# Kernel optimization log

Hardware: AMD Instinct MI355X
Metric: run time of the kernel (lower is better)

Reference implementation:

```python
import jax, jax.numpy as jnp
import numpy as np

B, L, T, H, NL, DFF, DIN = 4096, 64, 256, 8, 4, 1024, 6
HD = T // H
EPS = 1e-9


def setup_inputs() -> dict:
    key = jax.random.key(0)
    ks = jax.random.split(key, 12)
    s = 0.02
    inp = {
        "link_states": jax.random.uniform(ks[0], (B, L, DIN), jnp.float32) * 10.0,
        "link_W1": jax.random.normal(ks[1], (L, DIN, T), jnp.float32) * s,
        "link_b1": jnp.zeros((L, T), jnp.float32),
        "link_W2": jax.random.normal(ks[2], (L, T, T), jnp.float32) * s,
        "link_b2": jnp.zeros((L, T), jnp.float32),
        "Wqkv": jax.random.normal(ks[3], (NL, 3 * T, T), jnp.float32) * s,
        "bqkv": jnp.zeros((NL, 3 * T), jnp.float32),
        "Wo": jax.random.normal(ks[4], (NL, T, T), jnp.float32) * s,
        "bo": jnp.zeros((NL, T), jnp.float32),
        "ln1_g": jnp.ones((NL, T), jnp.float32),
        "ln1_b": jnp.zeros((NL, T), jnp.float32),
        "Wff1": jax.random.normal(ks[5], (NL, DFF, T), jnp.float32) * s,
        "bff1": jnp.zeros((NL, DFF), jnp.float32),
        "Wff2": jax.random.normal(ks[6], (NL, T, DFF), jnp.float32) * s,
        "bff2": jnp.zeros((NL, T), jnp.float32),
        "ln2_g": jnp.ones((NL, T), jnp.float32),
        "ln2_b": jnp.zeros((NL, T), jnp.float32),
        "head_W1": jax.random.normal(ks[7], (T, T), jnp.float32) * s,
        "head_b1": jnp.zeros((T,), jnp.float32),
        "head_W2": jax.random.normal(ks[8], (T, 1), jnp.float32) * s,
        "head_b2": jnp.zeros((1,), jnp.float32),
    }
    return inp


def _layernorm(x, g, b):
    m = x.mean(-1, keepdims=True)
    v = ((x - m) ** 2).mean(-1, keepdims=True)
    return (x - m) * jax.lax.rsqrt(v + 1e-5) * g + b


def _normalize_inputs(x):
    # x: [B, L, 6]
    prop = jnp.clip(x[:, :, 0], 0.0)
    tx = jnp.clip(x[:, :, 1], 0.0)
    sum_pt = prop + tx
    # torch.median returns lower-middle element for even L
    t_ref = jnp.sort(sum_pt, axis=1)[:, (L - 1) // 2][:, None]
    t_ref = jnp.clip(t_ref, 1e-6)
    f0 = prop / t_ref
    f1 = tx / t_ref
    f2 = x[:, :, 2]
    f3 = jnp.log1p(jnp.clip(x[:, :, 3], 0.0))
    f4 = jnp.log1p(jnp.clip(x[:, :, 4], 0.0) / t_ref)
    f5 = jnp.log1p(jnp.clip(x[:, :, 5], 0.0))
    head5 = jnp.stack([f0, f1, f2, f3, f4], axis=-1)  # [B,L,5]
    mean_a = head5.mean(axis=1, keepdims=True)
    std_a = head5.std(axis=1, keepdims=True) + EPS
    head5 = jnp.clip(head5, mean_a - 3.0 * std_a, mean_a + 3.0 * std_a)
    mean = head5.mean(axis=1, keepdims=True)
    std = head5.std(axis=1, keepdims=True) + EPS
    head5 = (head5 - mean) / std
    return jnp.concatenate([head5, f5[:, :, None]], axis=-1)


def _posenc():
    pos = jnp.arange(L, dtype=jnp.float32)[:, None]
    div = jnp.exp(-jnp.log(10000.0) * jnp.arange(0, T, 2, dtype=jnp.float32) / T)
    pe = jnp.zeros((L, T), jnp.float32)
    pe = pe.at[:, 0::2].set(jnp.sin(pos * div))
    pe = pe.at[:, 1::2].set(jnp.cos(pos * div))
    return pe


def _forward(link_states, link_W1, link_b1, link_W2, link_b2, Wqkv, bqkv, Wo, bo,
             ln1_g, ln1_b, Wff1, bff1, Wff2, bff2, ln2_g, ln2_b,
             head_W1, head_b1, head_W2, head_b2):
    x = _normalize_inputs(link_states)  # [B,L,6]
    # per-link (unshared) MLP encoders, batched as grouped matmuls
    h = jax.nn.relu(jnp.einsum('bld,ldt->blt', x, link_W1) + link_b1)
    tok = jnp.einsum('blt,lts->bls', h, link_W2) + link_b2  # [B,L,T]
    y = tok + _posenc()
    scale = 1.0 / np.sqrt(HD)
    for l in range(NL):
        qkv = y @ Wqkv[l].T + bqkv[l]  # [B,L,3T]
        q, k, v = jnp.split(qkv, 3, axis=-1)
        q = q.reshape(B, L, H, HD).transpose(0, 2, 1, 3)
        k = k.reshape(B, L, H, HD).transpose(0, 2, 1, 3)
        v = v.reshape(B, L, H, HD).transpose(0, 2, 1, 3)
        attn = jax.nn.softmax(jnp.einsum('bhqd,bhkd->bhqk', q, k) * scale, axis=-1)
        o = jnp.einsum('bhqk,bhkd->bhqd', attn, v).transpose(0, 2, 1, 3).reshape(B, L, T)
        o = o @ Wo[l].T + bo[l]
        y = _layernorm(y + o, ln1_g[l], ln1_b[l])
        ff = jax.nn.relu(y @ Wff1[l].T + bff1[l]) @ Wff2[l].T + bff2[l]
        y = _layernorm(y + ff, ln2_g[l], ln2_b[l])
    pooled = y.mean(axis=1)  # [B,T]
    hh = jax.nn.relu(pooled @ head_W1 + head_b1)
    values = (hh @ head_W2 + head_b2)[:, 0]  # [B]
    return values


def reference(link_states, link_W1, link_b1, link_W2, link_b2, Wqkv, bqkv, Wo, bo,
              ln1_g, ln1_b, Wff1, bff1, Wff2, bff2, ln2_g, ln2_b,
              head_W1, head_b1, head_W2, head_b2):
    return _forward(link_states, link_W1, link_b1, link_W2, link_b2, Wqkv, bqkv, Wo, bo,
                    ln1_g, ln1_b, Wff1, bff1, Wff2, bff2, ln2_g, ln2_b,
                    head_W1, head_b1, head_W2, head_b2)
```

## Files before the change

kernel.cpp:

```cpp
#include <hip/hip_runtime.h>
#include <cstddef>

#define B_   4096
#define L_   64
#define T_   256
#define H_   8
#define HD_  32
#define NL_  4
#define DFF_ 1024
#define DIN_ 6

typedef unsigned short ushort_t;
typedef __attribute__((ext_vector_type(8))) short bf16x8;
typedef __attribute__((ext_vector_type(4))) float f32x4;

__device__ __forceinline__ float wred_sum(float v) {
#pragma unroll
  for (int off = 32; off >= 1; off >>= 1) v += __shfl_xor(v, off, 64);
  return v;
}
__device__ __forceinline__ ushort_t f2bf(float f) {
  unsigned u = __builtin_bit_cast(unsigned, f);
  u += 0x7fffu + ((u >> 16) & 1u);
  return (ushort_t)(u >> 16);
}
__device__ __forceinline__ float bf2f(ushort_t h) {
  unsigned u = ((unsigned)h) << 16;
  return __builtin_bit_cast(float, u);
}
__device__ __forceinline__ void gl16(const ushort_t* g, const ushort_t* l) {
  __builtin_amdgcn_global_load_lds(
      (const __attribute__((address_space(1))) unsigned int*)g,
      (__attribute__((address_space(3))) unsigned int*)l, 16, 0, 0);
}

__global__ __launch_bounds__(64) void normalize_k(const float* __restrict__ xs,
                                                  float* __restrict__ xn) {
  const int b = blockIdx.x;
  const int l = threadIdx.x;
  const float* x = xs + ((size_t)b * L_ + l) * DIN_;
  const float x0 = x[0], x1 = x[1], x2 = x[2], x3 = x[3], x4 = x[4], x5 = x[5];
  const float prop = fmaxf(x0, 0.f), tx = fmaxf(x1, 0.f);
  const float sp = prop + tx;

  __shared__ float sh[64];
  __shared__ float med_sh;
  sh[l] = sp;
  __syncthreads();
  int rk = 0;
#pragma unroll 8
  for (int j = 0; j < 64; ++j) {
    const float vj = sh[j];
    rk += (vj < sp) || (vj == sp && j < l);
  }
  if (rk == 31) med_sh = sp;
  __syncthreads();
  const float t_ref = fmaxf(med_sh, 1e-6f);

  float f[5];
  f[0] = prop / t_ref;
  f[1] = tx / t_ref;
  f[2] = x2;
  f[3] = log1pf(fmaxf(x3, 0.f));
  f[4] = log1pf(fmaxf(x4, 0.f) / t_ref);
  const float f5 = log1pf(fmaxf(x5, 0.f));

  float* dst = xn + ((size_t)b * L_ + l) * DIN_;
#pragma unroll
  for (int i = 0; i < 5; ++i) {
    float v = f[i];
    float m = wred_sum(v) * (1.f / 64.f);
    float d = v - m;
    float sd = sqrtf(wred_sum(d * d) * (1.f / 64.f)) + 1e-9f;
    const float lo = m - 3.f * sd, hi = m + 3.f * sd;
    const float cv = fminf(fmaxf(v, lo), hi);
    const float m2 = wred_sum(cv) * (1.f / 64.f);
    const float d2 = cv - m2;
    const float sd2 = sqrtf(wred_sum(d2 * d2) * (1.f / 64.f)) + 1e-9f;
    dst[i] = (cv - m2) / sd2;
  }
  dst[5] = f5;
}

__global__ void pe_k(float* __restrict__ pe) {
  const int l = blockIdx.x;
  const int i = threadIdx.x;
  const float div = expf(-9.210340371976184f * (2.0f * i) / 256.0f);
  const float ang = (float)l * div;
  pe[l * T_ + 2 * i]     = sinf(ang);
  pe[l * T_ + 2 * i + 1] = cosf(ang);
}

__global__ void wfrag_k(const float* __restrict__ in, ushort_t* __restrict__ out,
                        int NK, int ksh) {
  const size_t z = blockIdx.z;
  const int idx = blockIdx.x * 256 + threadIdx.x;
  if (idx >= NK) return;
  const int e = idx & 7, li = (idx >> 3) & 15, t = idx >> 7;
  const int ks = t & ((1 << ksh) - 1), cb = t >> ksh;
  const int K = 8 << ksh;
  out[z * (size_t)NK + idx] =
      f2bf(in[z * (size_t)NK + (size_t)(cb * 16 + li) * K + ks * 8 + e]);
}

__global__ void w2t_k(const float* __restrict__ in, ushort_t* __restrict__ out) {
  const int idx = blockIdx.x * 256 + threadIdx.x;
  const int l = idx >> 16, r = idx & 65535, s = r >> 8, t = r & 255;
  out[idx] = f2bf(in[(l << 16) | (t << 8) | s]);
}

__global__ __launch_bounds__(256) void link1_k(const float* __restrict__ xn,
                                               const float* __restrict__ W1,
                                               const float* __restrict__ b1,
                                               ushort_t* __restrict__ h) {
  const size_t bl = blockIdx.x;
  const int l = (int)(bl & (L_ - 1));
  const int t = threadIdx.x;
  const float* x = xn + bl * DIN_;
  float a = b1[l * T_ + t];
#pragma unroll
  for (int d = 0; d < DIN_; ++d)
    a = fmaf(x[d], W1[((size_t)l * DIN_ + d) * T_ + t], a);
  h[bl * T_ + t] = f2bf(fmaxf(a, 0.f));
}

__global__ __launch_bounds__(512) void linkgemm_k(
    const ushort_t* __restrict__ A,
    const ushort_t* __restrict__ W,
    const float* __restrict__ bias,
    const float* __restrict__ pe,
    float* __restrict__ y32) {
  __shared__ ushort_t lA[2][4096];
  __shared__ ushort_t lB[2][8192];
  const int tid = threadIdx.x;
  const int lane = tid & 63, w = tid >> 6;
  const int wr = w >> 2, wc = w & 3;
  const size_t b0 = (size_t)blockIdx.x * 128;
  const int l = blockIdx.z;
  const ushort_t* Az = A + b0 * 16384 + (size_t)l * 256;
  const ushort_t* Wz = W + (size_t)l * 65536;

  const int sm = tid >> 6, sks = (tid >> 4) & 3, srr = tid & 15;

  auto stage = [&](int buf, int kt) {
    gl16(Az + (size_t)(16 * sm + srr) * 16384 + kt + sks * 8,
         &lA[buf][(tid & ~63) * 8]);
#pragma unroll
    for (int rd = 0; rd < 2; ++rd) {
      const int nb = sm + rd * 8;
      gl16(Wz + (size_t)(nb * 16 + srr) * 256 + kt + sks * 8,
           &lB[buf][rd * 4096 + (tid & ~63) * 8]);
    }
  };

  f32x4 acc[4][4];
#pragma unroll
  for (int mi = 0; mi < 4; ++mi)
#pragma unroll
    for (int ni = 0; ni < 4; ++ni) acc[mi][ni] = (f32x4){0.f, 0.f, 0.f, 0.f};

  stage(0, 0);
  asm volatile("s_waitcnt vmcnt(0)" ::: "memory");
  __syncthreads();
  int cur = 0;
  for (int t = 0; t < 8; ++t) {
    if (t + 1 < 8) stage(cur ^ 1, (t + 1) << 5);
    bf16x8 af[4], bfr[4];
#pragma unroll
    for (int mi = 0; mi < 4; ++mi)
      af[mi] = *(const bf16x8*)&lA[cur][((wr * 4 + mi) * 64 + lane) * 8];
#pragma unroll
    for (int ni = 0; ni < 4; ++ni)
      bfr[ni] = *(const bf16x8*)&lB[cur][((wc * 4 + ni) * 64 + lane) * 8];
#pragma unroll
    for (int mi = 0; mi < 4; ++mi)
#pragma unroll
      for (int ni = 0; ni < 4; ++ni)
        acc[mi][ni] = __builtin_amdgcn_mfma_f32_16x16x32_bf16(
            af[mi], bfr[ni], acc[mi][ni], 0, 0, 0);
    asm volatile("s_waitcnt vmcnt(0)" ::: "memory");
    __syncthreads();
    cur ^= 1;
  }

  const int r_in = (lane >> 4) * 4;
  const int c_in = lane & 15;
#pragma unroll
  for (int ni = 0; ni < 4; ++ni) {
    const int cg = wc * 64 + ni * 16 + c_in;
    const float bs = bias[l * 256 + cg] + pe[l * 256 + cg];
#pragma unroll
    for (int mi = 0; mi < 4; ++mi) {
#pragma unroll
      for (int rg = 0; rg < 4; ++rg) {
        const size_t bg = b0 + wr * 64 + mi * 16 + r_in + rg;
        y32[bg * 16384 + l * 256 + cg] = acc[mi][ni][rg] + bs;
      }
    }
  }
}

__global__ __launch_bounds__(256, 2) void layer_k(
    float* __restrict__ y32,
    const ushort_t* __restrict__ Wq, const float* __restrict__ bqkv,
    const ushort_t* __restrict__ Wo, const float* __restrict__ bo,
    const float* __restrict__ ln1g, const float* __restrict__ ln1b,
    const ushort_t* __restrict__ Wf1, const float* __restrict__ bf1,
    const ushort_t* __restrict__ Wf2, const float* __restrict__ bf2,
    const float* __restrict__ ln2g, const float* __restrict__ ln2b) {
  __shared__ ushort_t yF[16384];
  __shared__ ushort_t sc[18432];
  __shared__ float red[4][2][64];
  const int b = blockIdx.x;
  const int tid = threadIdx.x, lane = tid & 63, w = tid >> 6;
  const int li = lane & 15, g = lane >> 4;
  const size_t row0 = (size_t)b * 64;
  const float scale = 0.17677669529663687f;
  ushort_t* bufw = sc + w * 2304;
  ushort_t* vtw  = sc + 9216 + w * 2304;
  ushort_t* zF   = sc;

#pragma unroll
  for (int j = 0; j < 8; ++j) {
    const int u = j * 256 + tid;
    const int row = u & 63, ks = u >> 6;
    const float* src = y32 + (row0 + row) * 256 + ks * 8;
    const float4 a = *(const float4*)src;
    const float4 c = *(const float4*)(src + 4);
    uint2 pk;
    pk.x = (unsigned)f2bf(a.x) | ((unsigned)f2bf(a.y) << 16);
    pk.y = (unsigned)f2bf(a.z) | ((unsigned)f2bf(a.w) << 16);
    uint2 pk2;
    pk2.x = (unsigned)f2bf(c.x) | ((unsigned)f2bf(c.y) << 16);
    pk2.y = (unsigned)f2bf(c.z) | ((unsigned)f2bf(c.w) << 16);
    uint4 v = make_uint4(pk.x, pk.y, pk2.x, pk2.y);
    *(uint4*)&yF[(((row >> 4) * 32 + ks) * 16 + (row & 15)) * 8] = v;
  }
  __syncthreads();

  f32x4 oa2[2][4][2];
#pragma unroll
  for (int hi = 0; hi < 2; ++hi) {
    const int h = w * 2 + hi, hoff = h * 32;

    f32x4 acc[3][2][4];
#pragma unroll
    for (int m = 0; m < 3; ++m)
#pragma unroll
      for (int n = 0; n < 2; ++n)
#pragma unroll
        for (int mi = 0; mi < 4; ++mi) acc[m][n][mi] = (f32x4){0.f, 0.f, 0.f, 0.f};
#pragma unroll
    for (int kt = 0; kt < 8; ++kt) {
      bf16x8 af[4];
#pragma unroll
      for (int mi = 0; mi < 4; ++mi)
        af[mi] = *(const bf16x8*)&yF[((mi * 32 + kt * 4 + g) * 16 + li) * 8];
      bf16x8 bw[3][2];
#pragma unroll
      for (int m = 0; m < 3; ++m)
#pragma unroll
        for (int n = 0; n < 2; ++n)
          bw[m][n] = *(const bf16x8*)(Wq +
              (size_t)(((m * 16 + 2 * h + n) * 32 + kt * 4 + g) * 16 + li) * 8);
#pragma unroll
      for (int m = 0; m < 3; ++m)
#pragma unroll
        for (int n = 0; n < 2; ++n)
#pragma unroll
          for (int mi = 0; mi < 4; ++mi)
            acc[m][n][mi] = __builtin_amdgcn_mfma_f32_16x16x32_bf16(
                af[mi], bw[m][n], acc[m][n][mi], 0, 0, 0);
    }
    float bs[3][2];
#pragma unroll
    for (int m = 0; m < 3; ++m)
#pragma unroll
      for (int n = 0; n < 2; ++n) bs[m][n] = bqkv[m * 256 + hoff + 16 * n + li];

#pragma unroll
    for (int n = 0; n < 2; ++n)
#pragma unroll
      for (int mi = 0; mi < 4; ++mi)
#pragma unroll
        for (int r = 0; r < 4; ++r)
          bufw[(16 * mi + 4 * g + r) * 36 + 16 * n + li] =
              f2bf(acc[0][n][mi][r] + bs[0][n]);
    bf16x8 qb[4];
#pragma unroll
    for (int ni = 0; ni < 4; ++ni)
      qb[ni] = *(const bf16x8*)&bufw[(16 * ni + li) * 36 + g * 8];

#pragma unroll
    for (int n = 0; n < 2; ++n)
#pragma unroll
      for (int mi = 0; mi < 4; ++mi)
#pragma unroll
        for (int r = 0; r < 4; ++r)
          bufw[(16 * mi + 4 * g + r) * 36 + 16 * n + li] =
              f2bf(acc[1][n][mi][r] + bs[1][n]);
    bf16x8 ka[4];
#pragma unroll
    for (int mi = 0; mi < 4; ++mi)
      ka[mi] = *(const bf16x8*)&bufw[(16 * mi + li) * 36 + g * 8];

#pragma unroll
    for (int n = 0; n < 2; ++n)
#pragma unroll
      for (int mi = 0; mi < 4; ++mi)
#pragma unroll
        for (int r = 0; r < 4; ++r)
          vtw[(16 * n + li) * 72 + 16 * mi + 4 * g + r] =
              f2bf(acc[2][n][mi][r] + bs[2][n]);
    bf16x8 vb[2][2];
#pragma unroll
    for (int ks = 0; ks < 2; ++ks)
#pragma unroll
      for (int n2 = 0; n2 < 2; ++n2)
        vb[ks][n2] = *(const bf16x8*)&vtw[(16 * n2 + li) * 72 + ks * 32 + g * 8];

#pragma unroll
    for (int mi = 0; mi < 4; ++mi)
#pragma unroll
      for (int n2 = 0; n2 < 2; ++n2) oa2[hi][mi][n2] = (f32x4){0.f, 0.f, 0.f, 0.f};

#pragma unroll
    for (int half = 0; half < 2; ++half) {
      f32x4 s[4][2];
#pragma unroll
      for (int mi = 0; mi < 4; ++mi)
#pragma unroll
        for (int nn = 0; nn < 2; ++nn)
          s[mi][nn] = __builtin_amdgcn_mfma_f32_16x16x32_bf16(
              ka[mi], qb[2 * half + nn], (f32x4){0.f, 0.f, 0.f, 0.f}, 0, 0, 0);

#pragma unroll
      for (int nn = 0; nn < 2; ++nn) {
        float mx = -3.4e38f;
#pragma unroll
        for (int mi = 0; mi < 4; ++mi)
#pragma unroll
          for (int r = 0; r < 4; ++r) {
            s[mi][nn][r] *= scale;
            mx = fmaxf(mx, s[mi][nn][r]);
          }
        mx = fmaxf(mx, __shfl_xor(mx, 16, 64));
        mx = fmaxf(mx, __shfl_xor(mx, 32, 64));
        float sum = 0.f;
#pragma unroll
        for (int mi = 0; mi < 4; ++mi)
#pragma unroll
          for (int r = 0; r < 4; ++r) {
            const float e = expf(s[mi][nn][r] - mx);
            s[mi][nn][r] = e;
            sum += e;
          }
        sum += __shfl_xor(sum, 16, 64);
        sum += __shfl_xor(sum, 32, 64);
        const float inv = 1.f / sum;
        const int qrow = 16 * nn + li;
#pragma unroll
        for (int mi = 0; mi < 4; ++mi) {
          unsigned lo = (unsigned)f2bf(s[mi][nn][0] * inv) |
                        ((unsigned)f2bf(s[mi][nn][1] * inv) << 16);
          unsigned hi2 = (unsigned)f2bf(s[mi][nn][2] * inv) |
                         ((unsigned)f2bf(s[mi][nn][3] * inv) << 16);
          *(uint2*)&bufw[qrow * 72 + 16 * mi + 4 * g] = make_uint2(lo, hi2);
        }
      }

#pragma unroll
      for (int ks = 0; ks < 2; ++ks) {
        bf16x8 pa[2];
#pragma unroll
        for (int m2 = 0; m2 < 2; ++m2)
          pa[m2] = *(const bf16x8*)&bufw[(16 * m2 + li) * 72 + ks * 32 + g * 8];
#pragma unroll
        for (int m2 = 0; m2 < 2; ++m2)
#pragma unroll
          for (int n2 = 0; n2 < 2; ++n2)
            oa2[hi][2 * half + m2][n2] = __builtin_amdgcn_mfma_f32_16x16x32_bf16(
                pa[m2], vb[ks][n2], oa2[hi][2 * half + m2][n2], 0, 0, 0);
      }
    }
  }

  __syncthreads();
#pragma unroll
  for (int hi = 0; hi < 2; ++hi) {
    const int hoff = (2 * w + hi) * 32;
#pragma unroll
    for (int mi = 0; mi < 4; ++mi)
#pragma unroll
      for (int n2 = 0; n2 < 2; ++n2)
#pragma unroll
        for (int r = 0; r < 4; ++r) {
          const int row = 16 * mi + 4 * g + r;
          const int col = hoff + 16 * n2 + li;
          yF[(((row >> 4) * 32 + (col >> 3)) * 16 + (row & 15)) * 8 + (col & 7)] =
              f2bf(oa2[hi][mi][n2][r]);
        }
  }
  __syncthreads();

  f32x4 acc[4][4];
#pragma unroll
  for (int mi = 0; mi < 4; ++mi)
#pragma unroll
    for (int ni = 0; ni < 4; ++ni) acc[mi][ni] = (f32x4){0.f, 0.f, 0.f, 0.f};
#pragma unroll
  for (int kt = 0; kt < 8; ++kt) {
    bf16x8 af[4], bfr[4];
#pragma unroll
    for (int mi = 0; mi < 4; ++mi)
      af[mi] = *(const bf16x8*)&yF[((mi * 32 + kt * 4 + g) * 16 + li) * 8];
#pragma unroll
    for (int ni = 0; ni < 4; ++ni)
      bfr[ni] = *(const bf16x8*)(Wo +
          (size_t)(((4 * w + ni) * 32 + kt * 4 + g) * 16 + li) * 8);
#pragma unroll
    for (int mi = 0; mi < 4; ++mi)
#pragma unroll
      for (int ni = 0; ni < 4; ++ni)
        acc[mi][ni] = __builtin_amdgcn_mfma_f32_16x16x32_bf16(
            af[mi], bfr[ni], acc[mi][ni], 0, 0, 0);
  }

  const int r_in = (lane >> 4) * 4;
  const int c_in = lane & 15;
  float y1r[4][4][4];
#pragma unroll
  for (int mi = 0; mi < 4; ++mi) {
#pragma unroll
    for (int rg = 0; rg < 4; ++rg) {
      const int row_l = 16 * mi + r_in + rg;
      float s1 = 0.f, s2 = 0.f;
#pragma unroll
      for (int ni = 0; ni < 4; ++ni) {
        const int cg = 64 * w + 16 * ni + c_in;
        const float zv = acc[mi][ni][rg] + bo[cg] + y32[(row0 + row_l) * 256 + cg];
        acc[mi][ni][rg] = zv;
        s1 += zv;
        s2 += zv * zv;
      }
#pragma unroll
      for (int off = 1; off <= 8; off <<= 1) {
        s1 += __shfl_xor(s1, off, 64);
        s2 += __shfl_xor(s2, off, 64);
      }
      if (c_in == 0) {
        red[w][0][row_l] = s1;
        red[w][1][row_l] = s2;
      }
    }
  }
  __syncthreads();
#pragma unroll
  for (int mi = 0; mi < 4; ++mi) {
#pragma unroll
    for (int rg = 0; rg < 4; ++rg) {
      const int row_l = 16 * mi + r_in + rg;
      const float S1 = red[0][0][row_l] + red[1][0][row_l] + red[2][0][row_l] + red[3][0][row_l];
      const float S2 = red[0][1][row_l] + red[1][1][row_l] + red[2][1][row_l] + red[3][1][row_l];
      const float m = S1 * (1.f / 256.f);
      const float var = S2 * (1.f / 256.f) - m * m;
      const float rs = rsqrtf(var + 1e-5f);
#pragma unroll
      for (int ni = 0; ni < 4; ++ni) {
        const int cg = 64 * w + 16 * ni + c_in;
        const float v = (acc[mi][ni][rg] - m) * rs * ln1g[cg] + ln1b[cg];
        y1r[mi][ni][rg] = v;
        yF[(((row_l >> 4) * 32 + (cg >> 3)) * 16 + (row_l & 15)) * 8 + (cg & 7)] =
            f2bf(v);
      }
    }
  }
  __syncthreads();

  f32x4 acc2[4][4];
#pragma unroll
  for (int mi = 0; mi < 4; ++mi)
#pragma unroll
    for (int ni = 0; ni < 4; ++ni) acc2[mi][ni] = (f32x4){0.f, 0.f, 0.f, 0.f};

#pragma unroll 1
  for (int q = 0; q < 4; ++q) {
#pragma unroll 1
    for (int p = 0; p < 2; ++p) {
      f32x4 acc1[4][2];
#pragma unroll
      for (int mi = 0; mi < 4; ++mi)
#pragma unroll
        for (int n = 0; n < 2; ++n) acc1[mi][n] = (f32x4){0.f, 0.f, 0.f, 0.f};
#pragma unroll
      for (int kt = 0; kt < 8; ++kt) {
        bf16x8 af[4], bw[2];
#pragma unroll
        for (int mi = 0; mi < 4; ++mi)
          af[mi] = *(const bf16x8*)&yF[((mi * 32 + kt * 4 + g) * 16 + li) * 8];
#pragma unroll
        for (int n = 0; n < 2; ++n)
          bw[n] = *(const bf16x8*)(Wf1 +
              (size_t)(((16 * q + 4 * w + 2 * p + n) * 32 + kt * 4 + g) * 16 + li) * 8);
#pragma unroll
        for (int mi = 0; mi < 4; ++mi)
#pragma unroll
          for (int n = 0; n < 2; ++n)
            acc1[mi][n] = __builtin_amdgcn_mfma_f32_16x16x32_bf16(
                af[mi], bw[n], acc1[mi][n], 0, 0, 0);
      }
      if (q && p == 0) __syncthreads();
#pragma unroll
      for (int n = 0; n < 2; ++n) {
        const int kk = 64 * w + 32 * p + 16 * n + li;
        const float bb = bf1[256 * q + kk];
#pragma unroll
        for (int mi = 0; mi < 4; ++mi)
#pragma unroll
          for (int r = 0; r < 4; ++r) {
            const int row = 16 * mi + 4 * g + r;
            zF[(((row >> 4) * 32 + (kk >> 3)) * 16 + (row & 15)) * 8 + (kk & 7)] =
                f2bf(fmaxf(acc1[mi][n][r] + bb, 0.f));
          }
      }
    }
    __syncthreads();
#pragma unroll
    for (int kt = 0; kt < 8; ++kt) {
      bf16x8 af2[4], bw2[4];
#pragma unroll
      for (int mi = 0; mi < 4; ++mi)
        af2[mi] = *(const bf16x8*)&zF[((mi * 32 + kt * 4 + g) * 16 + li) * 8];
#pragma unroll
      for (int ni = 0; ni < 4; ++ni)
        bw2[ni] = *(const bf16x8*)(Wf2 +
            (size_t)(((4 * w + ni) * 128 + 32 * q + kt * 4 + g) * 16 + li) * 8);
#pragma unroll
      for (int mi = 0; mi < 4; ++mi)
#pragma unroll
        for (int ni = 0; ni < 4; ++ni)
          acc2[mi][ni] = __builtin_amdgcn_mfma_f32_16x16x32_bf16(
              af2[mi], bw2[ni], acc2[mi][ni], 0, 0, 0);
    }
  }

#pragma unroll
  for (int mi = 0; mi < 4; ++mi) {
#pragma unroll
    for (int rg = 0; rg < 4; ++rg) {
      const int row_l = 16 * mi + r_in + rg;
      float s1 = 0.f, s2 = 0.f;
#pragma unroll
      for (int ni = 0; ni < 4; ++ni) {
        const int cg = 64 * w + 16 * ni + c_in;
        const float zv = acc2[mi][ni][rg] + bf2[cg] + y1r[mi][ni][rg];
        acc2[mi][ni][rg] = zv;
        s1 += zv;
        s2 += zv * zv;
      }
#pragma unroll
      for (int off = 1; off <= 8; off <<= 1) {
        s1 += __shfl_xor(s1, off, 64);
        s2 += __shfl_xor(s2, off, 64);
      }
      if (c_in == 0) {
        red[w][0][row_l] = s1;
        red[w][1][row_l] = s2;
      }
    }
  }
  __syncthreads();
#pragma unroll
  for (int mi = 0; mi < 4; ++mi) {
#pragma unroll
    for (int rg = 0; rg < 4; ++rg) {
      const int row_l = 16 * mi + r_in + rg;
      const float S1 = red[0][0][row_l] + red[1][0][row_l] + red[2][0][row_l] + red[3][0][row_l];
      const float S2 = red[0][1][row_l] + red[1][1][row_l] + red[2][1][row_l] + red[3][1][row_l];
      const float m = S1 * (1.f / 256.f);
      const float var = S2 * (1.f / 256.f) - m * m;
      const float rs = rsqrtf(var + 1e-5f);
#pragma unroll
      for (int ni = 0; ni < 4; ++ni) {
        const int cg = 64 * w + 16 * ni + c_in;
        y32[(row0 + row_l) * 256 + cg] =
            (acc2[mi][ni][rg] - m) * rs * ln2g[cg] + ln2b[cg];
      }
    }
  }
}

__global__ __launch_bounds__(256) void pooled_k(const float* __restrict__ y,
                                                float* __restrict__ pooled) {
  const size_t b = blockIdx.x;
  const int t = threadIdx.x;
  const float* p = y + b * (L_ * T_) + t;
  float s = 0.f;
#pragma unroll
  for (int l = 0; l < L_; ++l) s += p[l * T_];
  pooled[b * T_ + t] = s * (1.f / 64.f);
}

__global__ __launch_bounds__(256) void headgemm_k(
    const float* __restrict__ A, const float* __restrict__ Wt,
    const float* __restrict__ bias, float* __restrict__ out) {
  const int tid = threadIdx.x;
  const int tx = tid & 63, ty = tid >> 6;
  const int cfull = tx * 4;
  const size_t b0 = (size_t)blockIdx.x * 64;

  __shared__ float At[256][68];

  float4 acc[16];
#pragma unroll
  for (int r = 0; r < 16; ++r) acc[r] = make_float4(0.f, 0.f, 0.f, 0.f);
  const int r0 = ty * 16;

  {
    const int rr = tid >> 6;
    const int k4 = (tid & 63) * 4;
#pragma unroll
    for (int p = 0; p < 16; ++p) {
      const int r = p * 4 + rr;
      const float4 v = *(const float4*)(A + (b0 + r) * 256 + k4);
      At[k4 + 0][r] = v.x;
      At[k4 + 1][r] = v.y;
      At[k4 + 2][r] = v.z;
      At[k4 + 3][r] = v.w;
    }
  }
  __syncthreads();
  const float* wp = Wt + cfull;
#pragma unroll 2
  for (int k = 0; k < 256; ++k) {
    const float4 w = *(const float4*)wp;
    wp += 256;
    const float4* ar = (const float4*)(&At[k][r0]);
    const float4 a0 = ar[0], a1 = ar[1], a2 = ar[2], a3 = ar[3];
    const float av[16] = {a0.x, a0.y, a0.z, a0.w, a1.x, a1.y, a1.z, a1.w,
                          a2.x, a2.y, a2.z, a2.w, a3.x, a3.y, a3.z, a3.w};
#pragma unroll
    for (int r = 0; r < 16; ++r) {
      acc[r].x = fmaf(av[r], w.x, acc[r].x);
      acc[r].y = fmaf(av[r], w.y, acc[r].y);
      acc[r].z = fmaf(av[r], w.z, acc[r].z);
      acc[r].w = fmaf(av[r], w.w, acc[r].w);
    }
  }
  const float4 bb = *(const float4*)(bias + cfull);
#pragma unroll
  for (int r = 0; r < 16; ++r) {
    const size_t row = b0 + r0 + r;
    float4 o;
    o.x = fmaxf(acc[r].x + bb.x, 0.f);
    o.y = fmaxf(acc[r].y + bb.y, 0.f);
    o.z = fmaxf(acc[r].z + bb.z, 0.f);
    o.w = fmaxf(acc[r].w + bb.w, 0.f);
    *(float4*)(out + row * 256 + cfull) = o;
  }
}

__global__ __launch_bounds__(64) void head2_k(const float* __restrict__ hh,
                                              const float* __restrict__ W2,
                                              const float* __restrict__ b2,
                                              float* __restrict__ out) {
  const size_t b = blockIdx.x;
  const int lane = threadIdx.x;
  const float4 hv = *(const float4*)(hh + b * T_ + lane * 4);
  const float4 wv = *(const float4*)(W2 + lane * 4);
  float s = hv.x * wv.x + hv.y * wv.y + hv.z * wv.z + hv.w * wv.w;
  s = wred_sum(s);
  if (lane == 0) out[b] = s + b2[0];
}

extern "C" void kernel_launch(void* const* d_in, const int* in_sizes, int n_in,
                              void* d_out, int out_size, void* d_ws, size_t ws_size,
                              hipStream_t stream) {
  const float* link_states = (const float*)d_in[0];
  const float* link_W1 = (const float*)d_in[1];
  const float* link_b1 = (const float*)d_in[2];
  const float* link_W2 = (const float*)d_in[3];
  const float* link_b2 = (const float*)d_in[4];
  const float* Wqkv = (const float*)d_in[5];
  const float* bqkv = (const float*)d_in[6];
  const float* Wo = (const float*)d_in[7];
  const float* bo = (const float*)d_in[8];
  const float* ln1_g = (const float*)d_in[9];
  const float* ln1_b = (const float*)d_in[10];
  const float* Wff1 = (const float*)d_in[11];
  const float* bff1 = (const float*)d_in[12];
  const float* Wff2 = (const float*)d_in[13];
  const float* bff2 = (const float*)d_in[14];
  const float* ln2_g = (const float*)d_in[15];
  const float* ln2_b = (const float*)d_in[16];
  const float* head_W1 = (const float*)d_in[17];
  const float* head_b1 = (const float*)d_in[18];
  const float* head_W2 = (const float*)d_in[19];
  const float* head_b2 = (const float*)d_in[20];

  char* base = (char*)d_ws;
  size_t off = 0;
  auto alloc = [&](size_t bytes) -> char* {
    char* p = base + off;
    off = (off + bytes + 255) & ~(size_t)255;
    return p;
  };

  ushort_t* Wqkv16 = (ushort_t*)alloc((size_t)NL_ * 768 * 256 * 2);
  ushort_t* Wo16   = (ushort_t*)alloc((size_t)NL_ * 256 * 256 * 2);
  ushort_t* Wff116 = (ushort_t*)alloc((size_t)NL_ * 1024 * 256 * 2);
  ushort_t* Wff216 = (ushort_t*)alloc((size_t)NL_ * 256 * 1024 * 2);
  ushort_t* W2T16  = (ushort_t*)alloc((size_t)L_ * 256 * 256 * 2);
  float* pe     = (float*)alloc((size_t)L_ * T_ * 4);
  float* xn     = (float*)alloc((size_t)B_ * L_ * DIN_ * 4);
  float* pooled = (float*)alloc((size_t)B_ * T_ * 4);
  float* hh     = (float*)alloc((size_t)B_ * T_ * 4);

  const size_t fixed_end = off;
  const size_t availB = (ws_size > fixed_end + 65536) ? (ws_size - fixed_end - 65536) : 0;
  int NC = 1;
  while (NC < 32 && (size_t)(B_ / NC) * 98304ull > availB) NC <<= 1;
  const int Bc = B_ / NC;

  float*    y32  = (float*)alloc((size_t)Bc * L_ * T_ * 4);
  ushort_t* hbuf = (ushort_t*)alloc((size_t)Bc * L_ * T_ * 2);

  wfrag_k<<<dim3((768 * 256 + 255) / 256, 1, NL_), 256, 0, stream>>>(
      Wqkv, Wqkv16, 768 * 256, 5);
  wfrag_k<<<dim3((256 * 256 + 255) / 256, 1, NL_), 256, 0, stream>>>(
      Wo, Wo16, 256 * 256, 5);
  wfrag_k<<<dim3((1024 * 256 + 255) / 256, 1, NL_), 256, 0, stream>>>(
      Wff1, Wff116, 1024 * 256, 5);
  wfrag_k<<<dim3((256 * 1024 + 255) / 256, 1, NL_), 256, 0, stream>>>(
      Wff2, Wff216, 256 * 1024, 7);
  w2t_k<<<(L_ * 256 * 256) / 256, 256, 0, stream>>>(link_W2, W2T16);
  pe_k<<<L_, 128, 0, stream>>>(pe);
  normalize_k<<<B_, 64, 0, stream>>>(link_states, xn);

  for (int c = 0; c < NC; ++c) {
    const size_t bs = (size_t)c * Bc;

    link1_k<<<Bc * L_, 256, 0, stream>>>(xn + bs * L_ * DIN_, link_W1, link_b1, hbuf);
    linkgemm_k<<<dim3(Bc / 128, 1, L_), 512, 0, stream>>>(
        hbuf, W2T16, link_b2, pe, y32);

    for (int l = 0; l < NL_; ++l) {
      layer_k<<<dim3(Bc, 1, 1), 256, 0, stream>>>(
          y32,
          Wqkv16 + (size_t)l * 768 * 256, bqkv + l * 768,
          Wo16 + (size_t)l * 256 * 256, bo + l * 256,
          ln1_g + l * 256, ln1_b + l * 256,
          Wff116 + (size_t)l * 1024 * 256, bff1 + l * 1024,
          Wff216 + (size_t)l * 256 * 1024, bff2 + l * 256,
          ln2_g + l * 256, ln2_b + l * 256);
    }

    pooled_k<<<Bc, 256, 0, stream>>>(y32, pooled + bs * T_);
  }

  headgemm_k<<<B_ / 64, 256, 0, stream>>>(pooled, head_W1, head_b1, hh);
  head2_k<<<B_, 64, 0, stream>>>(hh, head_W2, head_b2, (float*)d_out);
}
```

Before: 3.712 ms.

## Cut LDS and registers in layer kernel to fit three blocks per CU

Shrinks the per-block scratch LDS by half, reusing one per-wave buffer for V-transpose, Q and K staging. The FFN intermediate is now chunked in 128-column slices instead of 256, so the zF staging area fits in the smaller buffer. The fp32 y1 residual is no longer held in registers and is reread from the bf16 LDS copy, and launch bounds are raised to 3 blocks per CU to increase occupancy. In exchange there are more barriers in the FFN loop, and the second residual now uses bf16-rounded values, which reduces accuracy.

```diff
diff --git a/kernel.cpp b/kernel.cpp
--- a/kernel.cpp
+++ b/kernel.cpp
@@ -200,7 +200,7 @@
   }
 }
 
-__global__ __launch_bounds__(256, 2) void layer_k(
+__global__ __launch_bounds__(256, 3) void layer_k(
     float* __restrict__ y32,
     const ushort_t* __restrict__ Wq, const float* __restrict__ bqkv,
     const ushort_t* __restrict__ Wo, const float* __restrict__ bo,
@@ -209,7 +209,7 @@
     const ushort_t* __restrict__ Wf2, const float* __restrict__ bf2,
     const float* __restrict__ ln2g, const float* __restrict__ ln2b) {
   __shared__ ushort_t yF[16384];
-  __shared__ ushort_t sc[18432];
+  __shared__ ushort_t sc[9216];
   __shared__ float red[4][2][64];
   const int b = blockIdx.x;
   const int tid = threadIdx.x, lane = tid & 63, w = tid >> 6;
@@ -217,7 +217,6 @@
   const size_t row0 = (size_t)b * 64;
   const float scale = 0.17677669529663687f;
   ushort_t* bufw = sc + w * 2304;
-  ushort_t* vtw  = sc + 9216 + w * 2304;
   ushort_t* zF   = sc;
 
 #pragma unroll
@@ -227,13 +226,11 @@
     const float* src = y32 + (row0 + row) * 256 + ks * 8;
     const float4 a = *(const float4*)src;
     const float4 c = *(const float4*)(src + 4);
-    uint2 pk;
-    pk.x = (unsigned)f2bf(a.x) | ((unsigned)f2bf(a.y) << 16);
-    pk.y = (unsigned)f2bf(a.z) | ((unsigned)f2bf(a.w) << 16);
-    uint2 pk2;
-    pk2.x = (unsigned)f2bf(c.x) | ((unsigned)f2bf(c.y) << 16);
-    pk2.y = (unsigned)f2bf(c.z) | ((unsigned)f2bf(c.w) << 16);
-    uint4 v = make_uint4(pk.x, pk.y, pk2.x, pk2.y);
+    uint4 v;
+    v.x = (unsigned)f2bf(a.x) | ((unsigned)f2bf(a.y) << 16);
+    v.y = (unsigned)f2bf(a.z) | ((unsigned)f2bf(a.w) << 16);
+    v.z = (unsigned)f2bf(c.x) | ((unsigned)f2bf(c.y) << 16);
+    v.w = (unsigned)f2bf(c.z) | ((unsigned)f2bf(c.w) << 16);
     *(uint4*)&yF[(((row >> 4) * 32 + ks) * 16 + (row & 15)) * 8] = v;
   }
   __syncthreads();
@@ -277,6 +274,21 @@
     for (int m = 0; m < 3; ++m)
 #pragma unroll
       for (int n = 0; n < 2; ++n) bs[m][n] = bqkv[m * 256 + hoff + 16 * n + li];
+
+#pragma unroll
+    for (int n = 0; n < 2; ++n)
+#pragma unroll
+      for (int mi = 0; mi < 4; ++mi)
+#pragma unroll
+        for (int r = 0; r < 4; ++r)
+          bufw[(16 * n + li) * 72 + 16 * mi + 4 * g + r] =
+              f2bf(acc[2][n][mi][r] + bs[2][n]);
+    bf16x8 vb[2][2];
+#pragma unroll
+    for (int ks = 0; ks < 2; ++ks)
+#pragma unroll
+      for (int n2 = 0; n2 < 2; ++n2)
+        vb[ks][n2] = *(const bf16x8*)&bufw[(16 * n2 + li) * 72 + ks * 32 + g * 8];
 
 #pragma unroll
     for (int n = 0; n < 2; ++n)
@@ -303,21 +315,6 @@
 #pragma unroll
     for (int mi = 0; mi < 4; ++mi)
       ka[mi] = *(const bf16x8*)&bufw[(16 * mi + li) * 36 + g * 8];
-
-#pragma unroll
-    for (int n = 0; n < 2; ++n)
-#pragma unroll
-      for (int mi = 0; mi < 4; ++mi)
-#pragma unroll
-        for (int r = 0; r < 4; ++r)
-          vtw[(16 * n + li) * 72 + 16 * mi + 4 * g + r] =
-              f2bf(acc[2][n][mi][r] + bs[2][n]);
-    bf16x8 vb[2][2];
-#pragma unroll
-    for (int ks = 0; ks < 2; ++ks)
-#pragma unroll
-      for (int n2 = 0; n2 < 2; ++n2)
-        vb[ks][n2] = *(const bf16x8*)&vtw[(16 * n2 + li) * 72 + ks * 32 + g * 8];
 
 #pragma unroll
     for (int mi = 0; mi < 4; ++mi)
@@ -428,7 +425,6 @@
 
   const int r_in = (lane >> 4) * 4;
   const int c_in = lane & 15;
-  float y1r[4][4][4];
 #pragma unroll
   for (int mi = 0; mi < 4; ++mi) {
 #pragma unroll
@@ -469,7 +465,6 @@
       for (int ni = 0; ni < 4; ++ni) {
         const int cg = 64 * w + 16 * ni + c_in;
         const float v = (acc[mi][ni][rg] - m) * rs * ln1g[cg] + ln1b[cg];
-        y1r[mi][ni][rg] = v;
         yF[(((row_l >> 4) * 32 + (cg >> 3)) * 16 + (row_l & 15)) * 8 + (cg & 7)] =
             f2bf(v);
       }
@@ -484,57 +479,54 @@
     for (int ni = 0; ni < 4; ++ni) acc2[mi][ni] = (f32x4){0.f, 0.f, 0.f, 0.f};
 
 #pragma unroll 1
-  for (int q = 0; q < 4; ++q) {
-#pragma unroll 1
-    for (int p = 0; p < 2; ++p) {
-      f32x4 acc1[4][2];
-#pragma unroll
-      for (int mi = 0; mi < 4; ++mi)
-#pragma unroll
-        for (int n = 0; n < 2; ++n) acc1[mi][n] = (f32x4){0.f, 0.f, 0.f, 0.f};
-#pragma unroll
-      for (int kt = 0; kt < 8; ++kt) {
-        bf16x8 af[4], bw[2];
-#pragma unroll
-        for (int mi = 0; mi < 4; ++mi)
-          af[mi] = *(const bf16x8*)&yF[((mi * 32 + kt * 4 + g) * 16 + li) * 8];
+  for (int q8 = 0; q8 < 8; ++q8) {
+    f32x4 acc1[4][2];
+#pragma unroll
+    for (int mi = 0; mi < 4; ++mi)
+#pragma unroll
+      for (int n = 0; n < 2; ++n) acc1[mi][n] = (f32x4){0.f, 0.f, 0.f, 0.f};
+#pragma unroll
+    for (int kt = 0; kt < 8; ++kt) {
+      bf16x8 af[4], bw[2];
+#pragma unroll
+      for (int mi = 0; mi < 4; ++mi)
+        af[mi] = *(const bf16x8*)&yF[((mi * 32 + kt * 4 + g) * 16 + li) * 8];
+#pragma unroll
+      for (int n = 0; n < 2; ++n)
+        bw[n] = *(const bf16x8*)(Wf1 +
+            (size_t)(((8 * q8 + 2 * w + n) * 32 + kt * 4 + g) * 16 + li) * 8);
+#pragma unroll
+      for (int mi = 0; mi < 4; ++mi)
 #pragma unroll
         for (int n = 0; n < 2; ++n)
-          bw[n] = *(const bf16x8*)(Wf1 +
-              (size_t)(((16 * q + 4 * w + 2 * p + n) * 32 + kt * 4 + g) * 16 + li) * 8);
-#pragma unroll
-        for (int mi = 0; mi < 4; ++mi)
-#pragma unroll
-          for (int n = 0; n < 2; ++n)
-            acc1[mi][n] = __builtin_amdgcn_mfma_f32_16x16x32_bf16(
-                af[mi], bw[n], acc1[mi][n], 0, 0, 0);
-      }
-      if (q && p == 0) __syncthreads();
-#pragma unroll
-      for (int n = 0; n < 2; ++n) {
-        const int kk = 64 * w + 32 * p + 16 * n + li;
-        const float bb = bf1[256 * q + kk];
-#pragma unroll
-        for (int mi = 0; mi < 4; ++mi)
-#pragma unroll
-          for (int r = 0; r < 4; ++r) {
-            const int row = 16 * mi + 4 * g + r;
-            zF[(((row >> 4) * 32 + (kk >> 3)) * 16 + (row & 15)) * 8 + (kk & 7)] =
-                f2bf(fmaxf(acc1[mi][n][r] + bb, 0.f));
-          }
-      }
+          acc1[mi][n] = __builtin_amdgcn_mfma_f32_16x16x32_bf16(
+              af[mi], bw[n], acc1[mi][n], 0, 0, 0);
+    }
+    if (q8) __syncthreads();
+#pragma unroll
+    for (int n = 0; n < 2; ++n) {
+      const int kk = 32 * w + 16 * n + li;
+      const float bb = bf1[128 * q8 + kk];
+#pragma unroll
+      for (int mi = 0; mi < 4; ++mi)
+#pragma unroll
+        for (int r = 0; r < 4; ++r) {
+          const int row = 16 * mi + 4 * g + r;
+          zF[(((row >> 4) * 16 + (kk >> 3)) * 16 + (row & 15)) * 8 + (kk & 7)] =
+              f2bf(fmaxf(acc1[mi][n][r] + bb, 0.f));
+        }
     }
     __syncthreads();
 #pragma unroll
-    for (int kt = 0; kt < 8; ++kt) {
+    for (int kt = 0; kt < 4; ++kt) {
       bf16x8 af2[4], bw2[4];
 #pragma unroll
       for (int mi = 0; mi < 4; ++mi)
-        af2[mi] = *(const bf16x8*)&zF[((mi * 32 + kt * 4 + g) * 16 + li) * 8];
+        af2[mi] = *(const bf16x8*)&zF[((mi * 16 + kt * 4 + g) * 16 + li) * 8];
 #pragma unroll
       for (int ni = 0; ni < 4; ++ni)
         bw2[ni] = *(const bf16x8*)(Wf2 +
-            (size_t)(((4 * w + ni) * 128 + 32 * q + kt * 4 + g) * 16 + li) * 8);
+            (size_t)(((4 * w + ni) * 128 + 16 * q8 + kt * 4 + g) * 16 + li) * 8);
 #pragma unroll
       for (int mi = 0; mi < 4; ++mi)
 #pragma unroll
@@ -553,7 +545,9 @@
 #pragma unroll
       for (int ni = 0; ni < 4; ++ni) {
         const int cg = 64 * w + 16 * ni + c_in;
-        const float zv = acc2[mi][ni][rg] + bf2[cg] + y1r[mi][ni][rg];
+        const float y1v = bf2f(
+            yF[(((row_l >> 4) * 32 + (cg >> 3)) * 16 + (row_l & 15)) * 8 + (cg & 7)]);
+        const float zv = acc2[mi][ni][rg] + bf2[cg] + y1v;
         acc2[mi][ni][rg] = zv;
         s1 += zv;
         s2 += zv * zv;
```

Measured after the change: 4.956 ms. +33.5%, slower.
